# Kernel tuning notes

Hardware: AMD Instinct MI355X
Metric: run time of the kernel (lower is better)

Reference implementation:

```python
import jax, jax.numpy as jnp
import numpy as np

S, N, MSA_DIM, PAIR_DIM, D, H = 8, 256, 256, 128, 32, 8
EPS = 1e-5


def layer_norm(x, w, b):
    mu = jnp.mean(x, axis=-1, keepdims=True)
    var = jnp.mean((x - mu) ** 2, axis=-1, keepdims=True)
    return (x - mu) * jax.lax.rsqrt(var + EPS) * w + b


def setup_inputs() -> dict:
    key = jax.random.key(0)
    ks = jax.random.split(key, 8)
    def rnd(k, shape, scale=1.0):
        return jax.random.normal(k, shape, jnp.float32) * scale
    return {
        "msa_rep": rnd(ks[0], (S, N, MSA_DIM)),
        "pair_rep": rnd(ks[1], (N, N, PAIR_DIM)),
        "ln_w": jnp.ones((MSA_DIM,), jnp.float32),
        "ln_b": jnp.zeros((MSA_DIM,), jnp.float32),
        "w_qkv": rnd(ks[2], (MSA_DIM, 3 * H * D), 0.02),
        "ln_pair_w": jnp.ones((PAIR_DIM,), jnp.float32),
        "ln_pair_b": jnp.zeros((PAIR_DIM,), jnp.float32),
        "w_b": rnd(ks[3], (PAIR_DIM, H), 0.02),
        "w_g": rnd(ks[4], (MSA_DIM, H * D), 0.02),
        "w_out": rnd(ks[5], (H * D, MSA_DIM), 0.02),
        "b_out": jnp.zeros((MSA_DIM,), jnp.float32),
    }


def reference(msa_rep, pair_rep, ln_w, ln_b, w_qkv, ln_pair_w, ln_pair_b,
              w_b, w_g, w_out, b_out):
    s, n, _ = msa_rep.shape
    x = layer_norm(msa_rep, ln_w, ln_b)                      # [s, n, msa_dim]
    qkv = x @ w_qkv                                          # [s, n, 3*h*d]
    # chunk(3, dim=-1) then view(..., d, h): d outer, h inner
    q, k, v = [t.reshape(s, n, D, H) for t in jnp.split(qkv, 3, axis=-1)]
    # pair bias: LN + linear -> [n, n, h], broadcast to [1, i, j, 1, h]
    b = layer_norm(pair_rep, ln_pair_w, ln_pair_b) @ w_b     # [n, n, h]
    g = jax.nn.sigmoid(x @ w_g).reshape(s, n, D, H)          # gate [s, n, d, h]
    # NOTE: logits keep the d axis (no contraction): einsum 'sidh,sjdh->sijdh'
    scores = (q[:, :, None, :, :] * k[:, None, :, :, :]) * (D ** -0.5) \
             + b[None, :, :, None, :]                        # [s, i, j, d, h]
    a = jax.nn.softmax(scores, axis=2)                       # softmax over j
    out = g * jnp.einsum('sijdh,sjdh->sidh', a, v)           # [s, n, d, h]
    return out.reshape(s, n, D * H) @ w_out + b_out          # [s, n, msa_dim]
```

## Files before the change

### kernel.cpp

```cpp
#include <hip/hip_runtime.h>
#include <math.h>

#define S_DIM 8
#define N_RES 256
#define MSA_DIM 256
#define PAIR_DIM 128
#define D_DIM 32
#define H_DIM 8
#define M_ROWS (S_DIM * N_RES)
#define QKV_N (3 * H_DIM * D_DIM)
#define HD (H_DIM * D_DIM)

#define DPP_ADD(x, ctrl, rmask)                                                \
    x += __int_as_float(__builtin_amdgcn_update_dpp(                           \
        0, __float_as_int(x), (ctrl), (rmask), 0xf, true))

__device__ __forceinline__ float wave_sum63(float x) {
    DPP_ADD(x, 0x111, 0xf);
    DPP_ADD(x, 0x112, 0xf);
    DPP_ADD(x, 0x114, 0xf);
    DPP_ADD(x, 0x118, 0xf);
    DPP_ADD(x, 0x142, 0xa);
    DPP_ADD(x, 0x143, 0xc);
    return x;
}

__device__ __forceinline__ float quad_sum(float x) {
    x += __int_as_float(__builtin_amdgcn_update_dpp(
        0, __float_as_int(x), 0xB1, 0xf, 0xf, true));
    x += __int_as_float(__builtin_amdgcn_update_dpp(
        0, __float_as_int(x), 0x4E, 0xf, 0xf, true));
    return x;
}

__global__ __launch_bounds__(256) void ln_msa_kernel(
    const float* __restrict__ msa, const float* __restrict__ w,
    const float* __restrict__ b, float* __restrict__ x)
{
    int row = blockIdx.x;
    int t = threadIdx.x;
    float v = msa[row * MSA_DIM + t];
    float s1 = wave_sum63(v);
    float s2 = wave_sum63(v * v);
    __shared__ float r1[4], r2[4];
    int wave = t >> 6, lane = t & 63;
    if (lane == 63) { r1[wave] = s1; r2[wave] = s2; }
    __syncthreads();
    float S1 = r1[0] + r1[1] + r1[2] + r1[3];
    float S2 = r2[0] + r2[1] + r2[2] + r2[3];
    float mu = S1 * (1.0f / 256.0f);
    float var = S2 * (1.0f / 256.0f) - mu * mu;
    float rs = rsqrtf(var + 1e-5f);
    x[row * MSA_DIM + t] = (v - mu) * rs * w[t] + b[t];
}

__global__ __launch_bounds__(256) void xw_kernel(
    const float* __restrict__ X, const float* __restrict__ Wqkv,
    const float* __restrict__ Wg, float* __restrict__ q_t,
    float* __restrict__ k_t, float* __restrict__ v_t, float* __restrict__ g_t)
{
    __shared__ float Xs[16][68];
    __shared__ float Ws[16][64];
    int t = threadIdx.x;
    int bx = blockIdx.x;
    int qkv_mode = (bx < 12);
    const float* W = qkv_mode ? Wqkv : Wg;
    int Ncols = qkv_mode ? QKV_N : HD;
    int n0 = qkv_mode ? bx * 64 : (bx - 12) * 64;
    int m0 = blockIdx.y * 64;
    int tm = t >> 4, tn = t & 15;
    int lxm = t >> 2, lxk = (t & 3) * 4;
    int lwk = t >> 4, lwn = (t & 15) * 4;
    float acc[4][4] = {};
    for (int k0 = 0; k0 < 256; k0 += 16) {
        float4 xa = *(const float4*)&X[(m0 + lxm) * 256 + k0 + lxk];
        float4 wa = *(const float4*)&W[(k0 + lwk) * Ncols + n0 + lwn];
        __syncthreads();
        Xs[lxk + 0][lxm] = xa.x; Xs[lxk + 1][lxm] = xa.y;
        Xs[lxk + 2][lxm] = xa.z; Xs[lxk + 3][lxm] = xa.w;
        *(float4*)&Ws[lwk][lwn] = wa;
        __syncthreads();
#pragma unroll
        for (int kk = 0; kk < 16; kk++) {
            float4 a4 = *(const float4*)&Xs[kk][tm * 4];
            float4 b4 = *(const float4*)&Ws[kk][tn * 4];
            acc[0][0] += a4.x * b4.x; acc[0][1] += a4.x * b4.y; acc[0][2] += a4.x * b4.z; acc[0][3] += a4.x * b4.w;
            acc[1][0] += a4.y * b4.x; acc[1][1] += a4.y * b4.y; acc[1][2] += a4.y * b4.z; acc[1][3] += a4.y * b4.w;
            acc[2][0] += a4.z * b4.x; acc[2][1] += a4.z * b4.y; acc[2][2] += a4.z * b4.z; acc[2][3] += a4.z * b4.w;
            acc[3][0] += a4.w * b4.x; acc[3][1] += a4.w * b4.y; acc[3][2] += a4.w * b4.z; acc[3][3] += a4.w * b4.w;
        }
    }
#pragma unroll
    for (int ii = 0; ii < 4; ii++) {
#pragma unroll
        for (int jj = 0; jj < 4; jj++) {
            float c = acc[ii][jj];
            int mm = m0 + tm * 4 + ii;
            int nn = n0 + tn * 4 + jj;
            if (qkv_mode) {
                int chunk = nn >> 8, r = nn & 255, d = r >> 3, h = r & 7;
                float* dst = (chunk == 0) ? q_t : ((chunk == 1) ? k_t : v_t);
                dst[(h * M_ROWS + mm) * D_DIM + d] = c;
            } else {
                int d = nn >> 3, h = nn & 7;
                g_t[(h * M_ROWS + mm) * D_DIM + d] = 1.0f / (1.0f + __expf(-c));
            }
        }
    }
}

__global__ __launch_bounds__(256) void out_gemm_kernel(
    const float* __restrict__ X, const float* __restrict__ W,
    const float* __restrict__ bias, float* __restrict__ out)
{
    __shared__ float Xs[16][68];
    __shared__ float Ws[16][64];
    int t = threadIdx.x;
    int m0 = blockIdx.y * 64, n0 = blockIdx.x * 64;
    int tm = t >> 4, tn = t & 15;
    int lxm = t >> 2, lxk = (t & 3) * 4;
    int lwk = t >> 4, lwn = (t & 15) * 4;
    float acc[4][4] = {};
    for (int k0 = 0; k0 < 256; k0 += 16) {
        int k = k0 + lwk;
        int wrow = (k & 31) * 8 + (k >> 5);
        float4 xa = *(const float4*)&X[(m0 + lxm) * 256 + k0 + lxk];
        float4 wa = *(const float4*)&W[wrow * 256 + n0 + lwn];
        __syncthreads();
        Xs[lxk + 0][lxm] = xa.x; Xs[lxk + 1][lxm] = xa.y;
        Xs[lxk + 2][lxm] = xa.z; Xs[lxk + 3][lxm] = xa.w;
        *(float4*)&Ws[lwk][lwn] = wa;
        __syncthreads();
#pragma unroll
        for (int kk = 0; kk < 16; kk++) {
            float4 a4 = *(const float4*)&Xs[kk][tm * 4];
            float4 b4 = *(const float4*)&Ws[kk][tn * 4];
            acc[0][0] += a4.x * b4.x; acc[0][1] += a4.x * b4.y; acc[0][2] += a4.x * b4.z; acc[0][3] += a4.x * b4.w;
            acc[1][0] += a4.y * b4.x; acc[1][1] += a4.y * b4.y; acc[1][2] += a4.y * b4.z; acc[1][3] += a4.y * b4.w;
            acc[2][0] += a4.z * b4.x; acc[2][1] += a4.z * b4.y; acc[2][2] += a4.z * b4.z; acc[2][3] += a4.z * b4.w;
            acc[3][0] += a4.w * b4.x; acc[3][1] += a4.w * b4.y; acc[3][2] += a4.w * b4.z; acc[3][3] += a4.w * b4.w;
        }
    }
#pragma unroll
    for (int ii = 0; ii < 4; ii++) {
#pragma unroll
        for (int jj = 0; jj < 4; jj++) {
            int mm = m0 + tm * 4 + ii;
            int nn = n0 + tn * 4 + jj;
            out[mm * 256 + nn] = acc[ii][jj] + bias[nn];
        }
    }
}

__global__ __launch_bounds__(256) void pair_bias_kernel(
    const float* __restrict__ pair, const float* __restrict__ lw,
    const float* __restrict__ lb, const float* __restrict__ wb,
    float* __restrict__ b2)
{
    __shared__ float wbt[8][128];
    int t = threadIdx.x;
    for (int idx = t; idx < 1024; idx += 256) {
        int c = idx >> 3, h = idx & 7;
        wbt[h][c] = wb[idx];
    }
    __syncthreads();
    int wave = t >> 6, lane = t & 63;
    int row = blockIdx.x * 4 + wave;
    const float* in = pair + (size_t)row * PAIR_DIM;
    float x0 = in[lane], x1 = in[lane + 64];
    float s1 = wave_sum63(x0 + x1);
    float s2 = wave_sum63(x0 * x0 + x1 * x1);
    float S1 = __int_as_float(__builtin_amdgcn_readlane(__float_as_int(s1), 63));
    float S2 = __int_as_float(__builtin_amdgcn_readlane(__float_as_int(s2), 63));
    float mu = S1 * (1.0f / 128.0f);
    float var = S2 * (1.0f / 128.0f) - mu * mu;
    float rs = rsqrtf(var + 1e-5f);
    float xn0 = (x0 - mu) * rs * lw[lane] + lb[lane];
    float xn1 = (x1 - mu) * rs * lw[lane + 64] + lb[lane + 64];
    float ah[8];
#pragma unroll
    for (int h = 0; h < 8; h++) {
        float a = xn0 * wbt[h][lane] + xn1 * wbt[h][lane + 64];
        ah[h] = wave_sum63(a);
    }
    if (lane == 63) {
#pragma unroll
        for (int h = 0; h < 8; h++) b2[h * 65536 + row] = ah[h];
    }
}

__global__ __launch_bounds__(256) void attn_kernel(
    const float* __restrict__ q_t, const float* __restrict__ k_t,
    const float* __restrict__ v_t, const float* __restrict__ g_t,
    const float* __restrict__ b2, float* __restrict__ ao)
{
    __shared__ float k_sh[256][32];
    __shared__ float v_sh[256][32];
    int blk = blockIdx.x;
    int s = blk >> 6, h = (blk >> 3) & 7, it = blk & 7;
    int t = threadIdx.x;
    const float* kb = k_t + (size_t)(h * M_ROWS + s * N_RES) * D_DIM;
    const float* vb = v_t + (size_t)(h * M_ROWS + s * N_RES) * D_DIM;
    for (int idx = t; idx < 2048; idx += 256) {
        ((float4*)k_sh)[idx] = ((const float4*)kb)[idx];
        ((float4*)v_sh)[idx] = ((const float4*)vb)[idx];
    }
    __syncthreads();
    int jp = t & 3, dg = (t >> 2) & 7, li = t >> 5;
    int d0 = dg * 4;
    const float SCALE = 0.17677669529663687f;
    int ig[4], mrow[4];
    float qs[4][4];
#pragma unroll
    for (int r = 0; r < 4; r++) {
        ig[r] = it * 32 + r * 8 + li;
        mrow[r] = s * N_RES + ig[r];
        float4 q4 = *(const float4*)&q_t[(size_t)(h * M_ROWS + mrow[r]) * D_DIM + d0];
        qs[r][0] = q4.x * SCALE; qs[r][1] = q4.y * SCALE;
        qs[r][2] = q4.z * SCALE; qs[r][3] = q4.w * SCALE;
    }
    float den[4][4] = {}, acc[4][4] = {};
    const float* bbase = b2 + h * 65536;
    for (int js4 = 0; js4 < 16; js4++) {
        float bb[4][4];
#pragma unroll
        for (int r = 0; r < 4; r++)
            *(float4*)&bb[r][0] =
                *(const float4*)&bbase[ig[r] * 256 + jp * 64 + js4 * 4];
#pragma unroll
        for (int u = 0; u < 4; u++) {
            int j = jp * 64 + js4 * 4 + u;
            float ka[4], va[4];
            *(float4*)ka = *(const float4*)&k_sh[j][d0];
            *(float4*)va = *(const float4*)&v_sh[j][d0];
#pragma unroll
            for (int r = 0; r < 4; r++) {
#pragma unroll
                for (int c = 0; c < 4; c++) {
                    float e = __expf(qs[r][c] * ka[c] + bb[r][u]);
                    den[r][c] += e;
                    acc[r][c] += e * va[c];
                }
            }
        }
    }
#pragma unroll
    for (int r = 0; r < 4; r++)
#pragma unroll
        for (int c = 0; c < 4; c++) {
            den[r][c] = quad_sum(den[r][c]);
            acc[r][c] = quad_sum(acc[r][c]);
        }
    if (jp == 0) {
#pragma unroll
        for (int r = 0; r < 4; r++) {
            float4 g4 = *(const float4*)&g_t[(size_t)(h * M_ROWS + mrow[r]) * D_DIM + d0];
            float4 o;
            o.x = g4.x * acc[r][0] / den[r][0];
            o.y = g4.y * acc[r][1] / den[r][1];
            o.z = g4.z * acc[r][2] / den[r][2];
            o.w = g4.w * acc[r][3] / den[r][3];
            *(float4*)&ao[(size_t)mrow[r] * HD + h * 32 + d0] = o;
        }
    }
}

extern "C" void kernel_launch(void* const* d_in, const int* in_sizes, int n_in,
                              void* d_out, int out_size, void* d_ws, size_t ws_size,
                              hipStream_t stream)
{
    const float* msa_rep   = (const float*)d_in[0];
    const float* pair_rep  = (const float*)d_in[1];
    const float* ln_w      = (const float*)d_in[2];
    const float* ln_b      = (const float*)d_in[3];
    const float* w_qkv     = (const float*)d_in[4];
    const float* ln_pair_w = (const float*)d_in[5];
    const float* ln_pair_b = (const float*)d_in[6];
    const float* w_b       = (const float*)d_in[7];
    const float* w_g       = (const float*)d_in[8];
    const float* w_out     = (const float*)d_in[9];
    const float* b_out     = (const float*)d_in[10];
    float* out = (float*)d_out;

    float* ws = (float*)d_ws;
    const size_t CH = 524288;
    float* x   = ws + 0 * CH;
    float* q_t = ws + 1 * CH;
    float* k_t = ws + 2 * CH;
    float* v_t = ws + 3 * CH;
    float* g_t = ws + 4 * CH;
    float* b2  = ws + 5 * CH;
    float* ao  = ws + 6 * CH;

    ln_msa_kernel<<<M_ROWS, 256, 0, stream>>>(msa_rep, ln_w, ln_b, x);

    xw_kernel<<<dim3(16, M_ROWS / 64), 256, 0, stream>>>(
        x, w_qkv, w_g, q_t, k_t, v_t, g_t);

    pair_bias_kernel<<<65536 / 4, 256, 0, stream>>>(
        pair_rep, ln_pair_w, ln_pair_b, w_b, b2);

    attn_kernel<<<512, 256, 0, stream>>>(q_t, k_t, v_t, g_t, b2, ao);

    out_gemm_kernel<<<dim3(HD / 64, M_ROWS / 64), 256, 0, stream>>>(
        ao, w_out, b_out, out);
}
```

Measured before the change: 175.5 us.

## Fold pair LayerNorm into bias projection and use exp2 in attention

Adds a tiny setup kernel that folds the LayerNorm weight and bias and log2(e) into the pair-bias projection weights. The pair-bias kernel can then compute row statistics and the projection in a single pass with four threads per row instead of one wave per row, cutting wave-wide reductions and making the pair_rep reads vectorized. The attention kernel pre-scales q by log2(e) and calls the hardware exp2 directly, dropping a multiply inside the inner exp. The cost is one extra launch and a slight change in rounding.

```diff
diff --git a/kernel.cpp b/kernel.cpp
--- a/kernel.cpp
+++ b/kernel.cpp
@@ -10,6 +10,7 @@
 #define M_ROWS (S_DIM * N_RES)
 #define QKV_N (3 * H_DIM * D_DIM)
 #define HD (H_DIM * D_DIM)
+#define LOG2E 1.4426950408889634f
 
 #define DPP_ADD(x, ctrl, rmask)                                                \
     x += __int_as_float(__builtin_amdgcn_update_dpp(                           \
@@ -152,40 +153,77 @@
     }
 }
 
+__global__ __launch_bounds__(128) void pb_setup_kernel(
+    const float* __restrict__ lw, const float* __restrict__ lb,
+    const float* __restrict__ wb, float* __restrict__ Abuf)
+{
+    __shared__ float P[128][8], Q[128][8];
+    int c = threadIdx.x;
+    float lwc = lw[c], lbc = lb[c];
+#pragma unroll
+    for (int h = 0; h < 8; h++) {
+        float w = wb[c * 8 + h];
+        float a = lwc * w;
+        P[c][h] = a;
+        Q[c][h] = lbc * w;
+        Abuf[c * 12 + h] = a * LOG2E;
+    }
+    __syncthreads();
+    if (c < 8) {
+        float s = 0, cc = 0;
+        for (int k = 0; k < 128; k++) { s += P[k][c]; cc += Q[k][c]; }
+        Abuf[1536 + c] = s * LOG2E;
+        Abuf[1544 + c] = cc * LOG2E;
+    }
+}
+
 __global__ __launch_bounds__(256) void pair_bias_kernel(
-    const float* __restrict__ pair, const float* __restrict__ lw,
-    const float* __restrict__ lb, const float* __restrict__ wb,
+    const float* __restrict__ pair, const float* __restrict__ Abuf,
     float* __restrict__ b2)
 {
-    __shared__ float wbt[8][128];
-    int t = threadIdx.x;
-    for (int idx = t; idx < 1024; idx += 256) {
-        int c = idx >> 3, h = idx & 7;
-        wbt[h][c] = wb[idx];
-    }
+    __shared__ __align__(16) float As[1552];
+    int t = threadIdx.x;
+    for (int idx = t; idx < 388; idx += 256)
+        ((float4*)As)[idx] = ((const float4*)Abuf)[idx];
     __syncthreads();
-    int wave = t >> 6, lane = t & 63;
-    int row = blockIdx.x * 4 + wave;
+    int row = blockIdx.x * 64 + (t >> 2);
+    int q = t & 3;
     const float* in = pair + (size_t)row * PAIR_DIM;
-    float x0 = in[lane], x1 = in[lane + 64];
-    float s1 = wave_sum63(x0 + x1);
-    float s2 = wave_sum63(x0 * x0 + x1 * x1);
-    float S1 = __int_as_float(__builtin_amdgcn_readlane(__float_as_int(s1), 63));
-    float S2 = __int_as_float(__builtin_amdgcn_readlane(__float_as_int(s2), 63));
-    float mu = S1 * (1.0f / 128.0f);
-    float var = S2 * (1.0f / 128.0f) - mu * mu;
+    float4 x4[8];
+#pragma unroll
+    for (int it = 0; it < 8; it++)
+        x4[it] = *(const float4*)&in[it * 16 + q * 4];
+    float s = 0, s2 = 0;
+    float dot[8] = {};
+#pragma unroll
+    for (int it = 0; it < 8; it++) {
+        float xk[4];
+        *(float4*)xk = x4[it];
+#pragma unroll
+        for (int k = 0; k < 4; k++) {
+            int c = it * 16 + q * 4 + k;
+            float xv = xk[k];
+            s += xv; s2 += xv * xv;
+            float4 A0 = *(const float4*)&As[c * 12];
+            float4 A1 = *(const float4*)&As[c * 12 + 4];
+            dot[0] += xv * A0.x; dot[1] += xv * A0.y;
+            dot[2] += xv * A0.z; dot[3] += xv * A0.w;
+            dot[4] += xv * A1.x; dot[5] += xv * A1.y;
+            dot[6] += xv * A1.z; dot[7] += xv * A1.w;
+        }
+    }
+    s = quad_sum(s);
+    s2 = quad_sum(s2);
+#pragma unroll
+    for (int h = 0; h < 8; h++) dot[h] = quad_sum(dot[h]);
+    float mu = s * (1.0f / 128.0f);
+    float var = s2 * (1.0f / 128.0f) - mu * mu;
     float rs = rsqrtf(var + 1e-5f);
-    float xn0 = (x0 - mu) * rs * lw[lane] + lb[lane];
-    float xn1 = (x1 - mu) * rs * lw[lane + 64] + lb[lane + 64];
-    float ah[8];
-#pragma unroll
-    for (int h = 0; h < 8; h++) {
-        float a = xn0 * wbt[h][lane] + xn1 * wbt[h][lane + 64];
-        ah[h] = wave_sum63(a);
-    }
-    if (lane == 63) {
-#pragma unroll
-        for (int h = 0; h < 8; h++) b2[h * 65536 + row] = ah[h];
+    int h0 = q * 2;
+#pragma unroll
+    for (int u = 0; u < 2; u++) {
+        int h = h0 + u;
+        b2[h * 65536 + row] = rs * (dot[h] - mu * As[1536 + h]) + As[1544 + h];
     }
 }
 
@@ -208,7 +246,7 @@
     __syncthreads();
     int jp = t & 3, dg = (t >> 2) & 7, li = t >> 5;
     int d0 = dg * 4;
-    const float SCALE = 0.17677669529663687f;
+    const float SCL2 = 0.17677669529663687f * LOG2E;
     int ig[4], mrow[4];
     float qs[4][4];
 #pragma unroll
@@ -216,8 +254,8 @@
         ig[r] = it * 32 + r * 8 + li;
         mrow[r] = s * N_RES + ig[r];
         float4 q4 = *(const float4*)&q_t[(size_t)(h * M_ROWS + mrow[r]) * D_DIM + d0];
-        qs[r][0] = q4.x * SCALE; qs[r][1] = q4.y * SCALE;
-        qs[r][2] = q4.z * SCALE; qs[r][3] = q4.w * SCALE;
+        qs[r][0] = q4.x * SCL2; qs[r][1] = q4.y * SCL2;
+        qs[r][2] = q4.z * SCL2; qs[r][3] = q4.w * SCL2;
     }
     float den[4][4] = {}, acc[4][4] = {};
     const float* bbase = b2 + h * 65536;
@@ -237,7 +275,7 @@
             for (int r = 0; r < 4; r++) {
 #pragma unroll
                 for (int c = 0; c < 4; c++) {
-                    float e = __expf(qs[r][c] * ka[c] + bb[r][u]);
+                    float e = __builtin_amdgcn_exp2f(qs[r][c] * ka[c] + bb[r][u]);
                     den[r][c] += e;
                     acc[r][c] += e * va[c];
                 }
@@ -284,21 +322,23 @@
 
     float* ws = (float*)d_ws;
     const size_t CH = 524288;
-    float* x   = ws + 0 * CH;
-    float* q_t = ws + 1 * CH;
-    float* k_t = ws + 2 * CH;
-    float* v_t = ws + 3 * CH;
-    float* g_t = ws + 4 * CH;
-    float* b2  = ws + 5 * CH;
-    float* ao  = ws + 6 * CH;
+    float* x    = ws + 0 * CH;
+    float* q_t  = ws + 1 * CH;
+    float* k_t  = ws + 2 * CH;
+    float* v_t  = ws + 3 * CH;
+    float* g_t  = ws + 4 * CH;
+    float* b2   = ws + 5 * CH;
+    float* ao   = ws + 6 * CH;
+    float* Abuf = ws + 7 * CH;
 
     ln_msa_kernel<<<M_ROWS, 256, 0, stream>>>(msa_rep, ln_w, ln_b, x);
 
     xw_kernel<<<dim3(16, M_ROWS / 64), 256, 0, stream>>>(
         x, w_qkv, w_g, q_t, k_t, v_t, g_t);
 
-    pair_bias_kernel<<<65536 / 4, 256, 0, stream>>>(
-        pair_rep, ln_pair_w, ln_pair_b, w_b, b2);
+    pb_setup_kernel<<<1, 128, 0, stream>>>(ln_pair_w, ln_pair_b, w_b, Abuf);
+
+    pair_bias_kernel<<<65536 / 64, 256, 0, stream>>>(pair_rep, Abuf, b2);
 
     attn_kernel<<<512, 256, 0, stream>>>(q_t, k_t, v_t, g_t, b2, ao);
 
```

New measurement: 170.4 us. 2.9% less time.
